# Kernel optimization log

Measured on AMD Instinct MI355X. Metric: run time of the kernel, lower is better.

Reference implementation:

```python
import jax, jax.numpy as jnp
import numpy as np

D_MODEL = 256
D_K = 256
D_V = 256
B, S = 4, 4096


def setup_inputs() -> dict:
    key = jax.random.key(0)
    ks = jax.random.split(key, 9)
    q_in = jax.random.normal(ks[0], (B, S, D_MODEL), dtype=jnp.float32)
    k_in = jax.random.normal(ks[1], (B, S, D_MODEL), dtype=jnp.float32)
    v_in = jax.random.normal(ks[2], (B, S, D_MODEL), dtype=jnp.float32)
    # glorot-uniform-ish init for weights; biases small uniform (original uses glorot for bias too)
    lim_k = float(np.sqrt(6.0 / (D_MODEL + D_K)))
    lim_v = float(np.sqrt(6.0 / (D_MODEL + D_V)))
    Wq = jax.random.uniform(ks[3], (D_MODEL, D_K), minval=-lim_k, maxval=lim_k, dtype=jnp.float32)
    Wk = jax.random.uniform(ks[4], (D_MODEL, D_K), minval=-lim_k, maxval=lim_k, dtype=jnp.float32)
    Wv = jax.random.uniform(ks[5], (D_MODEL, D_V), minval=-lim_v, maxval=lim_v, dtype=jnp.float32)
    bq = jax.random.uniform(ks[6], (D_K,), minval=-lim_k, maxval=lim_k, dtype=jnp.float32)
    bk = jax.random.uniform(ks[7], (D_K,), minval=-lim_k, maxval=lim_k, dtype=jnp.float32)
    bv = jax.random.uniform(ks[8], (D_V,), minval=-lim_v, maxval=lim_v, dtype=jnp.float32)
    return {"q_in": q_in, "k_in": k_in, "v_in": v_in,
            "Wq": Wq, "bq": bq, "Wk": Wk, "bk": bk, "Wv": Wv, "bv": bv}


def reference(q_in, k_in, v_in, Wq, bq, Wk, bk, Wv, bv):
    # Dense projections on last dim
    q = jnp.einsum('bsd,dk->bsk', q_in, Wq) + bq  # [B,S,d_k]
    k = jnp.einsum('bsd,dk->bsk', k_in, Wk) + bk  # [B,S,d_k]
    v = jnp.einsum('bsd,dk->bsk', v_in, Wv) + bv  # [B,S,d_v]
    scale = 1.0 / jnp.sqrt(jnp.asarray(D_K, dtype=q.dtype))
    scores = jnp.einsum('bqk,bsk->bqs', q, k) * scale  # [B,S,S]
    attn = jax.nn.softmax(scores, axis=-1)
    return jnp.einsum('bqs,bsk->bqk', attn, v)  # [B,S,d_v]
```

## Files before the change

### kernel.cpp

```cpp
#include <hip/hip_runtime.h>
#include <hip/hip_bf16.h>
#include <stdint.h>

#define S_SZ 4096
#define SCL 0.09016844005586937f

typedef short bf16x8 __attribute__((ext_vector_type(8)));
typedef float f32x4 __attribute__((ext_vector_type(4)));
typedef float f32x16 __attribute__((ext_vector_type(16)));
typedef unsigned short u16;
typedef unsigned int u32;

#define MFMA16(a,b,c) __builtin_amdgcn_mfma_f32_16x16x32_bf16(a,b,c,0,0,0)
#define MFMA32(a,b,c) __builtin_amdgcn_mfma_f32_32x32x16_bf16(a,b,c,0,0,0)

__device__ __forceinline__ u32 cvtpk(float lo, float hi){
    u32 r;
    asm("v_cvt_pk_bf16_f32 %0, %1, %2" : "=v"(r) : "v"(lo), "v"(hi));
    return r;
}
__device__ __forceinline__ u16 cvt1(float a){ return (u16)cvtpk(a, a); }

__device__ __forceinline__ void async16(const void* g, void* l){
    __builtin_amdgcn_global_load_lds(
        (const __attribute__((address_space(1))) unsigned int*)g,
        (__attribute__((address_space(3))) unsigned int*)l, 16, 0, 0);
}

__global__ void wconv_kernel(const float* __restrict__ Wq, const float* __restrict__ Wk,
                             const float* __restrict__ Wv, u16* __restrict__ Wt){
    int idx = blockIdx.x*256 + threadIdx.x;
    int p = idx >> 16; int rem = idx & 65535;
    int dout = rem >> 8, din = rem & 255;
    const float* W = (p==0) ? Wq : ((p==1) ? Wk : Wv);
    Wt[idx] = cvt1(W[din*256 + dout]);
}

__global__ __launch_bounds__(256)
void proj_all_kernel(const float* __restrict__ Xq, const float* __restrict__ Xk,
                     const float* __restrict__ Xv, const u16* __restrict__ Wt,
                     const float* __restrict__ bq, const float* __restrict__ bk,
                     const float* __restrict__ bv,
                     u16* __restrict__ Qb, u16* __restrict__ Kb, u16* __restrict__ Vt){
    __shared__ char wlds[32768];
    int tid = threadIdx.x;
    int bid = blockIdx.x;
    int p = bid >> 8;
    const float* X    = (p==0) ? Xq : ((p==1) ? Xk : Xv);
    const float* bias = (p==0) ? bq : ((p==1) ? bk : bv);
    u16* Out          = (p==0) ? Qb : ((p==1) ? Kb : Vt);
    const char* Wbyte = (const char*)Wt + (size_t)p*131072;
    float scale = (p==0) ? SCL : 1.f;

    int w = tid >> 6, lane = tid & 63;
    int lr = lane & 15, lg = lane >> 4;
    int r0 = (bid & 255) * 64 + w * 16;

    bf16x8 a[8];
    #pragma unroll
    for (int ks = 0; ks < 8; ++ks){
        const float* src = X + (size_t)(r0 + lr)*256 + ks*32 + lg*8;
        float4 f0 = *(const float4*)src;
        float4 f1 = *(const float4*)(src+4);
        union { u32 wd[4]; bf16x8 v; } u;
        u.wd[0] = cvtpk(f0.x, f0.y);
        u.wd[1] = cvtpk(f0.z, f0.w);
        u.wd[2] = cvtpk(f1.x, f1.y);
        u.wd[3] = cvtpk(f1.z, f1.w);
        a[ks] = u.v;
    }

    for (int qtr = 0; qtr < 4; ++qtr){
        if (qtr) __syncthreads();
        const char* wsrc = Wbyte + qtr*32768;
        #pragma unroll
        for (int i = 0; i < 8; ++i){
            int o = i*4096 + tid*16;
            int dout = o >> 9, db = o & 511;
            async16(wsrc + ((dout<<9) | (db ^ ((dout&7)<<4))), wlds + o);
        }
        __syncthreads();

        #pragma unroll
        for (int dtl = 0; dtl < 4; ++dtl){
            int dt = qtr*4 + dtl;
            int dout_l = dtl*16 + lr;
            f32x4 acc = {0.f,0.f,0.f,0.f};
            #pragma unroll
            for (int ks = 0; ks < 8; ++ks){
                bf16x8 b = *(const bf16x8*)(wlds + dout_l*512 + ((ks*64 + lg*16) ^ ((dout_l&7)<<4)));
                acc = MFMA16(a[ks], b, acc);
            }
            float bv_ = bias[dt*16 + lr];
            int d = dt*16 + lr;
            if (p == 0){
                #pragma unroll
                for (int r = 0; r < 4; ++r){
                    int row = r0 + lg*4 + r;
                    Out[(size_t)row*256 + d] = cvt1((acc[r] + bv_)*scale);
                }
            } else if (p == 2){
                int row = r0 + lg*4;
                int bb = row >> 12;
                int s  = row & 4095;
                union { u32 wd[2]; ushort4 v; } u;
                u.wd[0] = cvtpk(acc[0]+bv_, acc[1]+bv_);
                u.wd[1] = cvtpk(acc[2]+bv_, acc[3]+bv_);
                u16* dst = Out + (size_t)bb*1048576 + (size_t)(s>>3)*2048 + d*8 + (s&7);
                *(ushort4*)dst = u.v;
            } else {
                int row = r0 + lg*4;
                int bb = row >> 12;
                int s  = row & 4095;
                u16* dst = Out + (size_t)bb*1048576 + (size_t)(d>>3)*32768 + (size_t)s*8 + (d&7);
                #pragma unroll
                for (int r = 0; r < 4; ++r)
                    dst[r*8] = cvt1(acc[r]+bv_);
            }
        }
    }
}

#define CH_ROWS 32
#define NCH     32

__global__ __launch_bounds__(256, 2)
void attn_kernel(const u16* __restrict__ Qb, const u16* __restrict__ Kb,
                 const u16* __restrict__ Vt, u16* __restrict__ Opart,
                 float* __restrict__ Mpart, float* __restrict__ Lpart){
    __shared__ char lds[65536];
    int tid = threadIdx.x;
    int w = tid >> 6, lane = tid & 63;
    int q5 = lane & 31, hi = lane >> 5;

    int bid = blockIdx.x;
    int xcd = bid & 7;
    int loc = bid >> 3;
    int combo = xcd*2 + (loc >> 5);
    int qb = loc & 31;
    int bb = combo >> 2;
    int split = combo & 3;
    int qrow0 = qb*128 + w*32;

    const char* Qbyte = (const char*)Qb + (size_t)bb*2097152;
    const char* Kbyte = (const char*)Kb + (size_t)bb*2097152;
    const char* Vbyte = (const char*)Vt + (size_t)bb*2097152;

    bf16x8 qf[16];
    #pragma unroll
    for (int c = 0; c < 16; ++c)
        qf[c] = *(const bf16x8*)(Qbyte + (size_t)(qrow0 + q5)*512 + c*32 + hi*16);

    f32x16 acc[8];
    #pragma unroll
    for (int dt=0;dt<8;++dt)
        #pragma unroll
        for (int i=0;i<16;++i) acc[dt][i] = 0.f;
    float m = -1e30f, ls = 0.f;

    int kv0 = split*1024;

    #pragma unroll
    for (int i = 0; i < 4; ++i){
        int o = i*4096 + tid*16;
        async16(Kbyte + ((size_t)(o>>9)*65536 + (size_t)kv0*16 + (o&511)), lds + o);
    }
    #pragma unroll
    for (int i = 0; i < 4; ++i){
        int o = i*4096 + tid*16;
        async16(Vbyte + (size_t)kv0*512 + o, lds + 32768 + o);
    }
    __syncthreads();

    int buf = 0;
    for (int ch = 0; ch < NCH; ++ch){
        if (ch < NCH-1){
            int kvn = kv0 + (ch+1)*CH_ROWS;
            char* Kn = lds + (buf^1)*16384;
            char* Vn = lds + 32768 + (buf^1)*16384;
            #pragma unroll
            for (int i = 0; i < 4; ++i){
                int o = i*4096 + tid*16;
                async16(Kbyte + ((size_t)(o>>9)*65536 + (size_t)kvn*16 + (o&511)), Kn + o);
            }
            #pragma unroll
            for (int i = 0; i < 4; ++i){
                int o = i*4096 + tid*16;
                async16(Vbyte + (size_t)kvn*512 + o, Vn + o);
            }
        }
        char* Kl = lds + buf*16384;
        char* Vl = lds + 32768 + buf*16384;

        f32x16 sc;
        #pragma unroll
        for (int i=0;i<16;++i) sc[i] = 0.f;
        __builtin_amdgcn_s_setprio(1);
        #pragma unroll
        for (int c = 0; c < 16; ++c){
            bf16x8 kf = *(const bf16x8*)(Kl + (2*c + hi)*512 + q5*16);
            sc = MFMA32(kf, qf[c], sc);
        }
        __builtin_amdgcn_s_setprio(0);

        bf16x8 vfp0 = *(const bf16x8*)(Vl + hi*4096 + q5*16);
        bf16x8 vfp1 = *(const bf16x8*)(Vl + hi*4096 + (32 + q5)*16);

        float x0 = fmaxf(sc[0], sc[1]),  x1 = fmaxf(sc[2], sc[3]);
        float x2 = fmaxf(sc[4], sc[5]),  x3 = fmaxf(sc[6], sc[7]);
        float x4 = fmaxf(sc[8], sc[9]),  x5 = fmaxf(sc[10], sc[11]);
        float x6 = fmaxf(sc[12], sc[13]),x7 = fmaxf(sc[14], sc[15]);
        float y0 = fmaxf(x0, x1), y1 = fmaxf(x2, x3);
        float y2 = fmaxf(x4, x5), y3 = fmaxf(x6, x7);
        float lmax = fmaxf(fmaxf(y0, y1), fmaxf(y2, y3));
        float pm = fmaxf(lmax, __shfl_xor(lmax, 32));
        if (__any(pm > m + 8.0f)){
            float mn = fmaxf(m, pm);
            float alpha = __builtin_amdgcn_exp2f(m - mn);
            m = mn;
            ls *= alpha;
            #pragma unroll
            for (int dt=0;dt<8;++dt) acc[dt] *= alpha;
        }
        float p[16];
        #pragma unroll
        for (int i=0;i<16;++i) p[i] = __builtin_amdgcn_exp2f(sc[i] - m);
        float s0 = (p[0]+p[1]) + (p[2]+p[3]);
        float s1 = (p[4]+p[5]) + (p[6]+p[7]);
        float s2 = (p[8]+p[9]) + (p[10]+p[11]);
        float s3 = (p[12]+p[13]) + (p[14]+p[15]);
        ls += (s0+s1) + (s2+s3);

        bf16x8 pf[2];
        #pragma unroll
        for (int h=0; h<2; ++h){
            const int o8 = h*8;
            u32 A0 = cvtpk(p[o8+0], p[o8+1]);
            u32 A1 = cvtpk(p[o8+2], p[o8+3]);
            u32 B0 = cvtpk(p[o8+4], p[o8+5]);
            u32 B1 = cvtpk(p[o8+6], p[o8+7]);
            u32 XA0 = __shfl_xor(A0, 32);
            u32 XA1 = __shfl_xor(A1, 32);
            u32 XB0 = __shfl_xor(B0, 32);
            u32 XB1 = __shfl_xor(B1, 32);
            union { u32 wd[4]; bf16x8 v; } u;
            u.wd[0] = hi ? XB0 : A0;
            u.wd[1] = hi ? XB1 : A1;
            u.wd[2] = hi ? B0  : XA0;
            u.wd[3] = hi ? B1  : XA1;
            pf[h] = u.v;
        }

        __builtin_amdgcn_s_setprio(1);
        acc[0] = MFMA32(vfp0, pf[0], acc[0]);
        acc[1] = MFMA32(vfp1, pf[0], acc[1]);
        #pragma unroll
        for (int dt=2; dt<8; ++dt){
            bf16x8 vf = *(const bf16x8*)(Vl + hi*4096 + (dt*32 + q5)*16);
            acc[dt] = MFMA32(vf, pf[0], acc[dt]);
        }
        #pragma unroll
        for (int dt=0; dt<8; ++dt){
            bf16x8 vf = *(const bf16x8*)(Vl + (2 + hi)*4096 + (dt*32 + q5)*16);
            acc[dt] = MFMA32(vf, pf[1], acc[dt]);
        }
        __builtin_amdgcn_s_setprio(0);

        __syncthreads();
        buf ^= 1;
    }

    float l = ls + __shfl_xor(ls, 32);

    size_t pbase = (size_t)(split*4 + bb)*S_SZ*256;
    u16* orow = Opart + pbase + (size_t)(qrow0 + q5)*256;
    #pragma unroll
    for (int dt=0; dt<8; ++dt){
        #pragma unroll
        for (int g=0; g<4; ++g){
            int d0 = dt*32 + g*8 + hi*4;
            union { u32 wd[2]; uint2 v; } u;
            u.wd[0] = cvtpk(acc[dt][4*g+0], acc[dt][4*g+1]);
            u.wd[1] = cvtpk(acc[dt][4*g+2], acc[dt][4*g+3]);
            *(uint2*)(orow + d0) = u.v;
        }
    }
    if (lane < 32){
        int row = qrow0 + q5;
        Mpart[(split*4+bb)*S_SZ + row] = m;
        Lpart[(split*4+bb)*S_SZ + row] = l;
    }
}

__device__ __forceinline__ float bf2f(u16 x){
    union { u32 u; float f; } v; v.u = ((u32)x) << 16; return v.f;
}
__global__ void combine_kernel(const u16* __restrict__ Opart, const float* __restrict__ Mpart,
                               const float* __restrict__ Lpart, float* __restrict__ out){
    int idx = blockIdx.x*256 + threadIdx.x;
    int d4 = (idx & 63)*4;
    int row = idx >> 6;
    int bb = row >> 12, srow = row & 4095;
    float m[4], lv[4];
    #pragma unroll
    for (int i=0;i<4;++i){
        m[i]  = Mpart[(i*4+bb)*S_SZ + srow];
        lv[i] = Lpart[(i*4+bb)*S_SZ + srow];
    }
    float M = fmaxf(fmaxf(m[0],m[1]), fmaxf(m[2],m[3]));
    float L = 0.f; float wt[4];
    #pragma unroll
    for (int i=0;i<4;++i){ wt[i] = __builtin_amdgcn_exp2f(m[i]-M); L += lv[i]*wt[i]; }
    float inv = 1.f/L;
    float ox=0.f, oy=0.f, oz=0.f, ow=0.f;
    #pragma unroll
    for (int i=0;i<4;++i){
        ushort4 oi = *(const ushort4*)(Opart + (size_t)(i*4+bb)*S_SZ*256 + (size_t)srow*256 + d4);
        ox += bf2f(oi.x)*wt[i]; oy += bf2f(oi.y)*wt[i];
        oz += bf2f(oi.z)*wt[i]; ow += bf2f(oi.w)*wt[i];
    }
    float4 o; o.x = ox*inv; o.y = oy*inv; o.z = oz*inv; o.w = ow*inv;
    *(float4*)(out + (size_t)row*256 + d4) = o;
}

extern "C" void kernel_launch(void* const* d_in, const int* in_sizes, int n_in,
                              void* d_out, int out_size, void* d_ws, size_t ws_size,
                              hipStream_t stream) {
    const float* q_in = (const float*)d_in[0];
    const float* k_in = (const float*)d_in[1];
    const float* v_in = (const float*)d_in[2];
    const float* Wq   = (const float*)d_in[3];
    const float* bq   = (const float*)d_in[4];
    const float* Wk   = (const float*)d_in[5];
    const float* bk   = (const float*)d_in[6];
    const float* Wv   = (const float*)d_in[7];
    const float* bv   = (const float*)d_in[8];

    char* ws = (char*)d_ws;
    u16*  Qb    = (u16*)ws;
    u16*  Kb    = (u16*)(ws + 8388608);
    u16*  Vt    = (u16*)(ws + 16777216);
    u16*  Wt    = (u16*)(ws + 25165824);
    u16*  Opart = (u16*)(ws + 33554432);
    float* Mpart = (float*)(ws + 67108864);
    float* Lpart = (float*)(ws + 67371008);
    float* out   = (float*)d_out;

    hipLaunchKernelGGL(wconv_kernel,    dim3(768),  dim3(256), 0, stream, Wq, Wk, Wv, Wt);
    hipLaunchKernelGGL(proj_all_kernel, dim3(768),  dim3(256), 0, stream,
                       q_in, k_in, v_in, Wt, bq, bk, bv, Qb, Kb, Vt);
    hipLaunchKernelGGL(attn_kernel,     dim3(512),  dim3(256), 0, stream, Qb, Kb, Vt, Opart, Mpart, Lpart);
    hipLaunchKernelGGL(combine_kernel,  dim3(4096), dim3(256), 0, stream, Opart, Mpart, Lpart, out);
}
```

Before: 121.5 us.

## Software-pipeline PV of previous chunk with QK of current chunk

```diff
diff --git a/kernel.cpp b/kernel.cpp
--- a/kernel.cpp
+++ b/kernel.cpp
@@ -128,7 +128,7 @@
 void attn_kernel(const u16* __restrict__ Qb, const u16* __restrict__ Kb,
                  const u16* __restrict__ Vt, u16* __restrict__ Opart,
                  float* __restrict__ Mpart, float* __restrict__ Lpart){
-    __shared__ char lds[65536];
+    __shared__ char lds[81920];
     int tid = threadIdx.x;
     int w = tid >> 6, lane = tid & 63;
     int q5 = lane & 31, hi = lane >> 5;
@@ -157,6 +157,7 @@
         #pragma unroll
         for (int i=0;i<16;++i) acc[dt][i] = 0.f;
     float m = -1e30f, ls = 0.f;
+    bf16x8 pf0, pf1;
 
     int kv0 = split*1024;
 
@@ -172,12 +173,94 @@
     }
     __syncthreads();
 
-    int buf = 0;
-    for (int ch = 0; ch < NCH; ++ch){
+    {
+        char* Kl = lds;
+        f32x16 sc;
+        #pragma unroll
+        for (int i=0;i<16;++i) sc[i] = 0.f;
+        __builtin_amdgcn_s_setprio(1);
+        #pragma unroll
+        for (int c = 0; c < 16; ++c){
+            bf16x8 kf = *(const bf16x8*)(Kl + (2*c + hi)*512 + q5*16);
+            sc = MFMA32(kf, qf[c], sc);
+        }
+        __builtin_amdgcn_s_setprio(0);
+
+        int kvn = kv0 + CH_ROWS;
+        #pragma unroll
+        for (int i = 0; i < 4; ++i){
+            int o = i*4096 + tid*16;
+            async16(Kbyte + ((size_t)(o>>9)*65536 + (size_t)kvn*16 + (o&511)), lds + 16384 + o);
+        }
+        #pragma unroll
+        for (int i = 0; i < 4; ++i){
+            int o = i*4096 + tid*16;
+            async16(Vbyte + (size_t)kvn*512 + o, lds + 49152 + o);
+        }
+
+        float x0 = fmaxf(sc[0], sc[1]),  x1 = fmaxf(sc[2], sc[3]);
+        float x2 = fmaxf(sc[4], sc[5]),  x3 = fmaxf(sc[6], sc[7]);
+        float x4 = fmaxf(sc[8], sc[9]),  x5 = fmaxf(sc[10], sc[11]);
+        float x6 = fmaxf(sc[12], sc[13]),x7 = fmaxf(sc[14], sc[15]);
+        float lmax = fmaxf(fmaxf(fmaxf(x0,x1), fmaxf(x2,x3)),
+                           fmaxf(fmaxf(x4,x5), fmaxf(x6,x7)));
+        m = fmaxf(lmax, __shfl_xor(lmax, 32));
+        float p[16];
+        #pragma unroll
+        for (int i=0;i<16;++i) p[i] = __builtin_amdgcn_exp2f(sc[i] - m);
+        ls = ((p[0]+p[1])+(p[2]+p[3])) + ((p[4]+p[5])+(p[6]+p[7]))
+           + ((p[8]+p[9])+(p[10]+p[11])) + ((p[12]+p[13])+(p[14]+p[15]));
+        {
+            u32 A0 = cvtpk(p[0],p[1]), A1 = cvtpk(p[2],p[3]);
+            u32 B0 = cvtpk(p[4],p[5]), B1 = cvtpk(p[6],p[7]);
+            u32 XA0 = __shfl_xor(A0, 32), XA1 = __shfl_xor(A1, 32);
+            u32 XB0 = __shfl_xor(B0, 32), XB1 = __shfl_xor(B1, 32);
+            union { u32 wd[4]; bf16x8 v; } uu;
+            uu.wd[0] = hi ? XB0 : A0;
+            uu.wd[1] = hi ? XB1 : A1;
+            uu.wd[2] = hi ? B0  : XA0;
+            uu.wd[3] = hi ? B1  : XA1;
+            pf0 = uu.v;
+        }
+        {
+            u32 A0 = cvtpk(p[8],p[9]),   A1 = cvtpk(p[10],p[11]);
+            u32 B0 = cvtpk(p[12],p[13]), B1 = cvtpk(p[14],p[15]);
+            u32 XA0 = __shfl_xor(A0, 32), XA1 = __shfl_xor(A1, 32);
+            u32 XB0 = __shfl_xor(B0, 32), XB1 = __shfl_xor(B1, 32);
+            union { u32 wd[4]; bf16x8 v; } uu;
+            uu.wd[0] = hi ? XB0 : A0;
+            uu.wd[1] = hi ? XB1 : A1;
+            uu.wd[2] = hi ? B0  : XA0;
+            uu.wd[3] = hi ? B1  : XA1;
+            pf1 = uu.v;
+        }
+        __syncthreads();
+    }
+
+    int kcur = 1;
+    int vp = 0, vc = 1, vn = 2;
+    for (int ch = 1; ch < NCH; ++ch){
+        char* Kl = lds + kcur*16384;
+        char* Vp = lds + 32768 + vp*16384;
+
+        f32x16 sc;
+        #pragma unroll
+        for (int i=0;i<16;++i) sc[i] = 0.f;
+        __builtin_amdgcn_s_setprio(1);
+        #pragma unroll
+        for (int c = 0; c < 16; ++c){
+            bf16x8 kf = *(const bf16x8*)(Kl + (2*c + hi)*512 + q5*16);
+            sc = MFMA32(kf, qf[c], sc);
+            int dt = c & 7;
+            bf16x8 vf = *(const bf16x8*)(Vp + (2*(c>>3) + hi)*4096 + (dt*32 + q5)*16);
+            acc[dt] = MFMA32(vf, (c < 8) ? pf0 : pf1, acc[dt]);
+        }
+        __builtin_amdgcn_s_setprio(0);
+
         if (ch < NCH-1){
             int kvn = kv0 + (ch+1)*CH_ROWS;
-            char* Kn = lds + (buf^1)*16384;
-            char* Vn = lds + 32768 + (buf^1)*16384;
+            char* Kn = lds + (kcur^1)*16384;
+            char* Vn = lds + 32768 + vn*16384;
             #pragma unroll
             for (int i = 0; i < 4; ++i){
                 int o = i*4096 + tid*16;
@@ -189,30 +272,13 @@
                 async16(Vbyte + (size_t)kvn*512 + o, Vn + o);
             }
         }
-        char* Kl = lds + buf*16384;
-        char* Vl = lds + 32768 + buf*16384;
-
-        f32x16 sc;
-        #pragma unroll
-        for (int i=0;i<16;++i) sc[i] = 0.f;
-        __builtin_amdgcn_s_setprio(1);
-        #pragma unroll
-        for (int c = 0; c < 16; ++c){
-            bf16x8 kf = *(const bf16x8*)(Kl + (2*c + hi)*512 + q5*16);
-            sc = MFMA32(kf, qf[c], sc);
-        }
-        __builtin_amdgcn_s_setprio(0);
-
-        bf16x8 vfp0 = *(const bf16x8*)(Vl + hi*4096 + q5*16);
-        bf16x8 vfp1 = *(const bf16x8*)(Vl + hi*4096 + (32 + q5)*16);
 
         float x0 = fmaxf(sc[0], sc[1]),  x1 = fmaxf(sc[2], sc[3]);
         float x2 = fmaxf(sc[4], sc[5]),  x3 = fmaxf(sc[6], sc[7]);
         float x4 = fmaxf(sc[8], sc[9]),  x5 = fmaxf(sc[10], sc[11]);
         float x6 = fmaxf(sc[12], sc[13]),x7 = fmaxf(sc[14], sc[15]);
-        float y0 = fmaxf(x0, x1), y1 = fmaxf(x2, x3);
-        float y2 = fmaxf(x4, x5), y3 = fmaxf(x6, x7);
-        float lmax = fmaxf(fmaxf(y0, y1), fmaxf(y2, y3));
+        float lmax = fmaxf(fmaxf(fmaxf(x0,x1), fmaxf(x2,x3)),
+                           fmaxf(fmaxf(x4,x5), fmaxf(x6,x7)));
         float pm = fmaxf(lmax, __shfl_xor(lmax, 32));
         if (__any(pm > m + 8.0f)){
             float mn = fmaxf(m, pm);
@@ -225,49 +291,50 @@
         float p[16];
         #pragma unroll
         for (int i=0;i<16;++i) p[i] = __builtin_amdgcn_exp2f(sc[i] - m);
-        float s0 = (p[0]+p[1]) + (p[2]+p[3]);
-        float s1 = (p[4]+p[5]) + (p[6]+p[7]);
-        float s2 = (p[8]+p[9]) + (p[10]+p[11]);
-        float s3 = (p[12]+p[13]) + (p[14]+p[15]);
-        ls += (s0+s1) + (s2+s3);
-
-        bf16x8 pf[2];
+        ls += ((p[0]+p[1])+(p[2]+p[3])) + ((p[4]+p[5])+(p[6]+p[7]))
+            + ((p[8]+p[9])+(p[10]+p[11])) + ((p[12]+p[13])+(p[14]+p[15]));
+        {
+            u32 A0 = cvtpk(p[0],p[1]), A1 = cvtpk(p[2],p[3]);
+            u32 B0 = cvtpk(p[4],p[5]), B1 = cvtpk(p[6],p[7]);
+            u32 XA0 = __shfl_xor(A0, 32), XA1 = __shfl_xor(A1, 32);
+            u32 XB0 = __shfl_xor(B0, 32), XB1 = __shfl_xor(B1, 32);
+            union { u32 wd[4]; bf16x8 v; } uu;
+            uu.wd[0] = hi ? XB0 : A0;
+            uu.wd[1] = hi ? XB1 : A1;
+            uu.wd[2] = hi ? B0  : XA0;
+            uu.wd[3] = hi ? B1  : XA1;
+            pf0 = uu.v;
+        }
+        {
+            u32 A0 = cvtpk(p[8],p[9]),   A1 = cvtpk(p[10],p[11]);
+            u32 B0 = cvtpk(p[12],p[13]), B1 = cvtpk(p[14],p[15]);
+            u32 XA0 = __shfl_xor(A0, 32), XA1 = __shfl_xor(A1, 32);
+            u32 XB0 = __shfl_xor(B0, 32), XB1 = __shfl_xor(B1, 32);
+            union { u32 wd[4]; bf16x8 v; } uu;
+            uu.wd[0] = hi ? XB0 : A0;
+            uu.wd[1] = hi ? XB1 : A1;
+            uu.wd[2] = hi ? B0  : XA0;
+            uu.wd[3] = hi ? B1  : XA1;
+            pf1 = uu.v;
+        }
+
+        __syncthreads();
+        kcur ^= 1;
+        int tmp = vp; vp = vc; vc = vn; vn = tmp;
+    }
+
+    {
+        char* Vp = lds + 32768 + vp*16384;
+        __builtin_amdgcn_s_setprio(1);
         #pragma unroll
         for (int h=0; h<2; ++h){
-            const int o8 = h*8;
-            u32 A0 = cvtpk(p[o8+0], p[o8+1]);
-            u32 A1 = cvtpk(p[o8+2], p[o8+3]);
-            u32 B0 = cvtpk(p[o8+4], p[o8+5]);
-            u32 B1 = cvtpk(p[o8+6], p[o8+7]);
-            u32 XA0 = __shfl_xor(A0, 32);
-            u32 XA1 = __shfl_xor(A1, 32);
-            u32 XB0 = __shfl_xor(B0, 32);
-            u32 XB1 = __shfl_xor(B1, 32);
-            union { u32 wd[4]; bf16x8 v; } u;
-            u.wd[0] = hi ? XB0 : A0;
-            u.wd[1] = hi ? XB1 : A1;
-            u.wd[2] = hi ? B0  : XA0;
-            u.wd[3] = hi ? B1  : XA1;
-            pf[h] = u.v;
-        }
-
-        __builtin_amdgcn_s_setprio(1);
-        acc[0] = MFMA32(vfp0, pf[0], acc[0]);
-        acc[1] = MFMA32(vfp1, pf[0], acc[1]);
-        #pragma unroll
-        for (int dt=2; dt<8; ++dt){
-            bf16x8 vf = *(const bf16x8*)(Vl + hi*4096 + (dt*32 + q5)*16);
-            acc[dt] = MFMA32(vf, pf[0], acc[dt]);
-        }
-        #pragma unroll
-        for (int dt=0; dt<8; ++dt){
-            bf16x8 vf = *(const bf16x8*)(Vl + (2 + hi)*4096 + (dt*32 + q5)*16);
-            acc[dt] = MFMA32(vf, pf[1], acc[dt]);
+            #pragma unroll
+            for (int dt=0; dt<8; ++dt){
+                bf16x8 vf = *(const bf16x8*)(Vp + (2*h + hi)*4096 + (dt*32 + q5)*16);
+                acc[dt] = MFMA32(vf, h ? pf1 : pf0, acc[dt]);
+            }
         }
         __builtin_amdgcn_s_setprio(0);
-
-        __syncthreads();
-        buf ^= 1;
     }
 
     float l = ls + __shfl_xor(ls, 32);
@@ -279,10 +346,10 @@
         #pragma unroll
         for (int g=0; g<4; ++g){
             int d0 = dt*32 + g*8 + hi*4;
-            union { u32 wd[2]; uint2 v; } u;
-            u.wd[0] = cvtpk(acc[dt][4*g+0], acc[dt][4*g+1]);
-            u.wd[1] = cvtpk(acc[dt][4*g+2], acc[dt][4*g+3]);
-            *(uint2*)(orow + d0) = u.v;
+            union { u32 wd[2]; uint2 v; } u2;
+            u2.wd[0] = cvtpk(acc[dt][4*g+0], acc[dt][4*g+1]);
+            u2.wd[1] = cvtpk(acc[dt][4*g+2], acc[dt][4*g+3]);
+            *(uint2*)(orow + d0) = u2.v;
         }
     }
     if (lane < 32){
```

New measurement: 122.2 us. No clear change (+0.6%).

## Use 512-thread attention blocks with a 4-slot, distance-2 K/V prefetch ring

Applied to the files above, without the earlier changes.

```diff
diff --git a/kernel.cpp b/kernel.cpp
--- a/kernel.cpp
+++ b/kernel.cpp
@@ -124,11 +124,11 @@
 #define CH_ROWS 32
 #define NCH     32
 
-__global__ __launch_bounds__(256, 2)
+__global__ __launch_bounds__(512, 2)
 void attn_kernel(const u16* __restrict__ Qb, const u16* __restrict__ Kb,
                  const u16* __restrict__ Vt, u16* __restrict__ Opart,
                  float* __restrict__ Mpart, float* __restrict__ Lpart){
-    __shared__ char lds[65536];
+    __shared__ char lds[131072];
     int tid = threadIdx.x;
     int w = tid >> 6, lane = tid & 63;
     int q5 = lane & 31, hi = lane >> 5;
@@ -136,11 +136,11 @@
     int bid = blockIdx.x;
     int xcd = bid & 7;
     int loc = bid >> 3;
-    int combo = xcd*2 + (loc >> 5);
-    int qb = loc & 31;
+    int combo = xcd*2 + (loc >> 4);
+    int qb = loc & 15;
     int bb = combo >> 2;
     int split = combo & 3;
-    int qrow0 = qb*128 + w*32;
+    int qrow0 = qb*256 + w*32;
 
     const char* Qbyte = (const char*)Qb + (size_t)bb*2097152;
     const char* Kbyte = (const char*)Kb + (size_t)bb*2097152;
@@ -150,6 +150,7 @@
     #pragma unroll
     for (int c = 0; c < 16; ++c)
         qf[c] = *(const bf16x8*)(Qbyte + (size_t)(qrow0 + q5)*512 + c*32 + hi*16);
+    asm volatile("s_waitcnt vmcnt(0)" ::: "memory");
 
     f32x16 acc[8];
     #pragma unroll
@@ -160,37 +161,36 @@
 
     int kv0 = split*1024;
 
-    #pragma unroll
-    for (int i = 0; i < 4; ++i){
-        int o = i*4096 + tid*16;
-        async16(Kbyte + ((size_t)(o>>9)*65536 + (size_t)kv0*16 + (o&511)), lds + o);
-    }
-    #pragma unroll
-    for (int i = 0; i < 4; ++i){
-        int o = i*4096 + tid*16;
-        async16(Vbyte + (size_t)kv0*512 + o, lds + 32768 + o);
-    }
-    __syncthreads();
-
-    int buf = 0;
+    auto STAGE = [&](int c){
+        char* Kd = lds + (c&3)*16384;
+        char* Vd = lds + 65536 + (c&3)*16384;
+        int kv = kv0 + c*CH_ROWS;
+        #pragma unroll
+        for (int i = 0; i < 2; ++i){
+            int o = i*8192 + tid*16;
+            async16(Kbyte + ((size_t)(o>>9)*65536 + (size_t)kv*16 + (o&511)), Kd + o);
+        }
+        #pragma unroll
+        for (int i = 0; i < 2; ++i){
+            int o = i*8192 + tid*16;
+            async16(Vbyte + (size_t)kv*512 + o, Vd + o);
+        }
+    };
+
+    STAGE(0);
+    STAGE(1);
+
     for (int ch = 0; ch < NCH; ++ch){
-        if (ch < NCH-1){
-            int kvn = kv0 + (ch+1)*CH_ROWS;
-            char* Kn = lds + (buf^1)*16384;
-            char* Vn = lds + 32768 + (buf^1)*16384;
-            #pragma unroll
-            for (int i = 0; i < 4; ++i){
-                int o = i*4096 + tid*16;
-                async16(Kbyte + ((size_t)(o>>9)*65536 + (size_t)kvn*16 + (o&511)), Kn + o);
-            }
-            #pragma unroll
-            for (int i = 0; i < 4; ++i){
-                int o = i*4096 + tid*16;
-                async16(Vbyte + (size_t)kvn*512 + o, Vn + o);
-            }
-        }
-        char* Kl = lds + buf*16384;
-        char* Vl = lds + 32768 + buf*16384;
+        if (ch + 2 < NCH) STAGE(ch + 2);
+        if (ch < NCH-2)       { asm volatile("s_waitcnt vmcnt(8)" ::: "memory"); }
+        else if (ch == NCH-2) { asm volatile("s_waitcnt vmcnt(4)" ::: "memory"); }
+        else                  { asm volatile("s_waitcnt vmcnt(0)" ::: "memory"); }
+        __builtin_amdgcn_sched_barrier(0);
+        __builtin_amdgcn_s_barrier();
+        __builtin_amdgcn_sched_barrier(0);
+
+        char* Kl = lds + (ch&3)*16384;
+        char* Vl = lds + 65536 + (ch&3)*16384;
 
         f32x16 sc;
         #pragma unroll
@@ -202,17 +202,13 @@
             sc = MFMA32(kf, qf[c], sc);
         }
         __builtin_amdgcn_s_setprio(0);
-
-        bf16x8 vfp0 = *(const bf16x8*)(Vl + hi*4096 + q5*16);
-        bf16x8 vfp1 = *(const bf16x8*)(Vl + hi*4096 + (32 + q5)*16);
 
         float x0 = fmaxf(sc[0], sc[1]),  x1 = fmaxf(sc[2], sc[3]);
         float x2 = fmaxf(sc[4], sc[5]),  x3 = fmaxf(sc[6], sc[7]);
         float x4 = fmaxf(sc[8], sc[9]),  x5 = fmaxf(sc[10], sc[11]);
         float x6 = fmaxf(sc[12], sc[13]),x7 = fmaxf(sc[14], sc[15]);
-        float y0 = fmaxf(x0, x1), y1 = fmaxf(x2, x3);
-        float y2 = fmaxf(x4, x5), y3 = fmaxf(x6, x7);
-        float lmax = fmaxf(fmaxf(y0, y1), fmaxf(y2, y3));
+        float lmax = fmaxf(fmaxf(fmaxf(x0,x1), fmaxf(x2,x3)),
+                           fmaxf(fmaxf(x4,x5), fmaxf(x6,x7)));
         float pm = fmaxf(lmax, __shfl_xor(lmax, 32));
         if (__any(pm > m + 8.0f)){
             float mn = fmaxf(m, pm);
@@ -225,49 +221,47 @@
         float p[16];
         #pragma unroll
         for (int i=0;i<16;++i) p[i] = __builtin_amdgcn_exp2f(sc[i] - m);
-        float s0 = (p[0]+p[1]) + (p[2]+p[3]);
-        float s1 = (p[4]+p[5]) + (p[6]+p[7]);
-        float s2 = (p[8]+p[9]) + (p[10]+p[11]);
-        float s3 = (p[12]+p[13]) + (p[14]+p[15]);
-        ls += (s0+s1) + (s2+s3);
-
-        bf16x8 pf[2];
-        #pragma unroll
-        for (int h=0; h<2; ++h){
-            const int o8 = h*8;
-            u32 A0 = cvtpk(p[o8+0], p[o8+1]);
-            u32 A1 = cvtpk(p[o8+2], p[o8+3]);
-            u32 B0 = cvtpk(p[o8+4], p[o8+5]);
-            u32 B1 = cvtpk(p[o8+6], p[o8+7]);
-            u32 XA0 = __shfl_xor(A0, 32);
-            u32 XA1 = __shfl_xor(A1, 32);
-            u32 XB0 = __shfl_xor(B0, 32);
-            u32 XB1 = __shfl_xor(B1, 32);
-            union { u32 wd[4]; bf16x8 v; } u;
-            u.wd[0] = hi ? XB0 : A0;
-            u.wd[1] = hi ? XB1 : A1;
-            u.wd[2] = hi ? B0  : XA0;
-            u.wd[3] = hi ? B1  : XA1;
-            pf[h] = u.v;
+        ls += ((p[0]+p[1])+(p[2]+p[3])) + ((p[4]+p[5])+(p[6]+p[7]))
+            + ((p[8]+p[9])+(p[10]+p[11])) + ((p[12]+p[13])+(p[14]+p[15]));
+
+        bf16x8 pf0, pf1;
+        {
+            u32 A0 = cvtpk(p[0],p[1]), A1 = cvtpk(p[2],p[3]);
+            u32 B0 = cvtpk(p[4],p[5]), B1 = cvtpk(p[6],p[7]);
+            u32 XA0 = __shfl_xor(A0, 32), XA1 = __shfl_xor(A1, 32);
+            u32 XB0 = __shfl_xor(B0, 32), XB1 = __shfl_xor(B1, 32);
+            union { u32 wd[4]; bf16x8 v; } uu;
+            uu.wd[0] = hi ? XB0 : A0;
+            uu.wd[1] = hi ? XB1 : A1;
+            uu.wd[2] = hi ? B0  : XA0;
+            uu.wd[3] = hi ? B1  : XA1;
+            pf0 = uu.v;
+        }
+        {
+            u32 A0 = cvtpk(p[8],p[9]),   A1 = cvtpk(p[10],p[11]);
+            u32 B0 = cvtpk(p[12],p[13]), B1 = cvtpk(p[14],p[15]);
+            u32 XA0 = __shfl_xor(A0, 32), XA1 = __shfl_xor(A1, 32);
+            u32 XB0 = __shfl_xor(B0, 32), XB1 = __shfl_xor(B1, 32);
+            union { u32 wd[4]; bf16x8 v; } uu;
+            uu.wd[0] = hi ? XB0 : A0;
+            uu.wd[1] = hi ? XB1 : A1;
+            uu.wd[2] = hi ? B0  : XA0;
+            uu.wd[3] = hi ? B1  : XA1;
+            pf1 = uu.v;
         }
 
         __builtin_amdgcn_s_setprio(1);
-        acc[0] = MFMA32(vfp0, pf[0], acc[0]);
-        acc[1] = MFMA32(vfp1, pf[0], acc[1]);
-        #pragma unroll
-        for (int dt=2; dt<8; ++dt){
+        #pragma unroll
+        for (int dt=0; dt<8; ++dt){
             bf16x8 vf = *(const bf16x8*)(Vl + hi*4096 + (dt*32 + q5)*16);
-            acc[dt] = MFMA32(vf, pf[0], acc[dt]);
+            acc[dt] = MFMA32(vf, pf0, acc[dt]);
         }
         #pragma unroll
         for (int dt=0; dt<8; ++dt){
             bf16x8 vf = *(const bf16x8*)(Vl + (2 + hi)*4096 + (dt*32 + q5)*16);
-            acc[dt] = MFMA32(vf, pf[1], acc[dt]);
+            acc[dt] = MFMA32(vf, pf1, acc[dt]);
         }
         __builtin_amdgcn_s_setprio(0);
-
-        __syncthreads();
-        buf ^= 1;
     }
 
     float l = ls + __shfl_xor(ls, 32);
@@ -279,10 +273,10 @@
         #pragma unroll
         for (int g=0; g<4; ++g){
             int d0 = dt*32 + g*8 + hi*4;
-            union { u32 wd[2]; uint2 v; } u;
-            u.wd[0] = cvtpk(acc[dt][4*g+0], acc[dt][4*g+1]);
-            u.wd[1] = cvtpk(acc[dt][4*g+2], acc[dt][4*g+3]);
-            *(uint2*)(orow + d0) = u.v;
+            union { u32 wd[2]; uint2 v; } u2;
+            u2.wd[0] = cvtpk(acc[dt][4*g+0], acc[dt][4*g+1]);
+            u2.wd[1] = cvtpk(acc[dt][4*g+2], acc[dt][4*g+3]);
+            *(uint2*)(orow + d0) = u2.v;
         }
     }
     if (lane < 32){
@@ -349,6 +343,6 @@
     hipLaunchKernelGGL(wconv_kernel,    dim3(768),  dim3(256), 0, stream, Wq, Wk, Wv, Wt);
     hipLaunchKernelGGL(proj_all_kernel, dim3(768),  dim3(256), 0, stream,
                        q_in, k_in, v_in, Wt, bq, bk, bv, Qb, Kb, Vt);
-    hipLaunchKernelGGL(attn_kernel,     dim3(512),  dim3(256), 0, stream, Qb, Kb, Vt, Opart, Mpart, Lpart);
+    hipLaunchKernelGGL(attn_kernel,     dim3(256),  dim3(512), 0, stream, Qb, Kb, Vt, Opart, Mpart, Lpart);
     hipLaunchKernelGGL(combine_kernel,  dim3(4096), dim3(256), 0, stream, Opart, Mpart, Lpart, out);
 }
```

After: 117.7 us. 1.03x faster.
